# Kernel optimization log

Measured on AMD Instinct MI355X. Metric: run time of the kernel, lower is better.

## Reference

```python
import jax, jax.numpy as jnp
import numpy as np

N = 50000   # nodes
E = 800000  # edges per layer
D = 128     # feature dim
H = 256     # mlp hidden
O = 3       # output dim


def setup_inputs() -> dict:
    key = jax.random.key(0)
    ks = jax.random.split(key, 16)
    def lin(k, fan_out, fan_in):
        s = 1.0 / np.sqrt(fan_in)
        kw, kb = jax.random.split(k)
        return (jax.random.uniform(kw, (fan_out, fan_in), jnp.float32, -s, s),
                jax.random.uniform(kb, (fan_out,), jnp.float32, -s, s))
    x = jax.random.normal(ks[0], (N, D), jnp.float32)
    edge_idx0 = jax.random.randint(ks[1], (2, E), 0, N, dtype=jnp.int64)
    edge_idx1 = jax.random.randint(ks[2], (2, E), 0, N, dtype=jnp.int64)
    Wl1, bl1 = lin(ks[3], D, D)   # SAGE layer1: lin_l (aggregated neighbors, with bias)
    Wr1, _ = lin(ks[4], D, D)     # SAGE layer1: lin_r (root, no bias)
    Wl2, bl2 = lin(ks[5], D, D)
    Wr2, _ = lin(ks[6], D, D)
    Ws, bs = lin(ks[7], D, D)     # skip_fc
    W1, b1 = lin(ks[8], H, D)     # mlp hidden
    W2, b2 = lin(ks[9], O, H)     # mlp out
    return dict(x=x, edge_idx0=edge_idx0, edge_idx1=edge_idx1,
                Wl1=Wl1, bl1=bl1, Wr1=Wr1, Wl2=Wl2, bl2=bl2, Wr2=Wr2,
                Ws=Ws, bs=bs, W1=W1, b1=b1, W2=W2, b2=b2)


def _sage(x, ei, Wl, bl, Wr):
    # PyG SAGEConv with mean aggregation: out = lin_l(mean_j x_j) + lin_r(x_i)
    src, dst = ei[0], ei[1]
    agg = jax.ops.segment_sum(x[src], dst, num_segments=N)          # [N, D] gather-scatter
    cnt = jax.ops.segment_sum(jnp.ones((ei.shape[1],), x.dtype), dst, num_segments=N)
    agg = agg / jnp.maximum(cnt, 1.0)[:, None]
    return agg @ Wl.T + bl + x @ Wr.T


def reference(x, edge_idx0, edge_idx1, Wl1, bl1, Wr1, Wl2, bl2, Wr2,
              Ws, bs, W1, b1, W2, b2):
    inp = x
    h = _sage(x, edge_idx0, Wl1, bl1, Wr1)
    h = _sage(h, edge_idx1, Wl2, bl2, Wr2)
    h = h + (inp @ Ws.T + bs)            # skip connection
    h = jax.nn.relu(h @ W1.T + b1)       # MLP head
    return h @ W2.T + b2                  # [N, 3]
```

## Files before the change

### kernel.cpp

```cpp
#include <hip/hip_runtime.h>
#include <hip/hip_bf16.h>


#define DD 128
#define SB 8
#define CH 4096
typedef unsigned short u16;
typedef __attribute__((ext_vector_type(8))) short short8;
typedef __attribute__((ext_vector_type(4))) float f32x4;

__device__ inline u16 f2bf(float f) {
    __hip_bfloat16 h = __float2bfloat16(f);
    u16 u;
    __builtin_memcpy(&u, &h, 2);
    return u;
}
__device__ inline unsigned pack2(float lo, float hi) {
    return (unsigned)f2bf(lo) | ((unsigned)f2bf(hi) << 16);
}
__device__ inline float bf_lo(unsigned u) { union { unsigned x; float f; } c; c.x = u << 16; return c.f; }
__device__ inline float bf_hi(unsigned u) { union { unsigned x; float f; } c; c.x = u & 0xffff0000u; return c.f; }

struct CastJobs {
    const float4* src[6];
    uint2* dst[6];
    int qstart[7];
};

__global__ __launch_bounds__(256) void hist1_kernel(CastJobs jb,
                                                    const int* __restrict__ dst0, int* __restrict__ h0,
                                                    const int* __restrict__ dst1, int* __restrict__ h1,
                                                    int e0, int e1, int nb, int P) {
    int bx = blockIdx.x;
    int t = threadIdx.x;
    if (bx >= P) {
        if (blockIdx.y == 0) {
            int q = (bx - P) * 256 + t;
            if (q < jb.qstart[6]) {
                int i = 0;
#pragma unroll
                for (int k = 1; k < 6; ++k) if (q >= jb.qstart[k]) i = k;
                int local = q - jb.qstart[i];
                float4 v = jb.src[i][local];
                jb.dst[i][local] = make_uint2(pack2(v.x, v.y), pack2(v.z, v.w));
            }
        }
        return;
    }
    int arr = blockIdx.y;
    const int* dst = arr ? dst1 : dst0;
    int* hist = arr ? h1 : h0;
    int e = arr ? e1 : e0;
    __shared__ int h[256];
    h[t] = 0;
    __syncthreads();
    int base = bx * CH;
    int hi = min(base + CH, e);
    for (int i = base + t; i < hi; i += 256) atomicAdd(&h[dst[i] >> SB], 1);
    __syncthreads();
    if (t < nb) hist[t * P + bx] = h[t];
}

__global__ __launch_bounds__(256) void rowsum_kernel(const int* __restrict__ h0, int* __restrict__ bs0,
                                                     const int* __restrict__ h1, int* __restrict__ bs1,
                                                     int P) {
    int arr = blockIdx.y;
    const int* hist = arr ? h1 : h0;
    int* bs = arr ? bs1 : bs0;
    int b = blockIdx.x;
    __shared__ int s[256];
    int t = threadIdx.x;
    s[t] = (t < P) ? hist[b * P + t] : 0;
    __syncthreads();
    for (int off = 128; off; off >>= 1) {
        if (t < off) s[t] += s[t + off];
        __syncthreads();
    }
    if (t == 0) bs[b] = s[0];
}

__global__ __launch_bounds__(256) void bscan_kernel(const int* __restrict__ bs0, int* __restrict__ bb0, int* __restrict__ rp0, int e0,
                                                    const int* __restrict__ bs1, int* __restrict__ bb1, int* __restrict__ rp1, int e1,
                                                    int nb, int n) {
    int arr = blockIdx.x;
    const int* bsum = arr ? bs1 : bs0;
    int* bb = arr ? bb1 : bb0;
    int* rp = arr ? rp1 : rp0;
    int E = arr ? e1 : e0;
    __shared__ int s[256];
    int t = threadIdx.x;
    int v = (t < nb) ? bsum[t] : 0;
    s[t] = v;
    __syncthreads();
    for (int off = 1; off < 256; off <<= 1) {
        int u = (t >= off) ? s[t - off] : 0;
        __syncthreads();
        s[t] += u;
        __syncthreads();
    }
    if (t < nb) bb[t] = s[t] - v;
    if (t == 0) { bb[nb] = E; rp[n] = E; }
}

__global__ __launch_bounds__(256) void offs_kernel(int* __restrict__ h0, const int* __restrict__ bb0,
                                                   int* __restrict__ h1, const int* __restrict__ bb1,
                                                   int P) {
    int arr = blockIdx.y;
    int* hist = arr ? h1 : h0;
    const int* bb = arr ? bb1 : bb0;
    int b = blockIdx.x;
    __shared__ int s[256];
    int t = threadIdx.x;
    int v = (t < P) ? hist[b * P + t] : 0;
    s[t] = v;
    __syncthreads();
    for (int off = 1; off < 256; off <<= 1) {
        int u = (t >= off) ? s[t - off] : 0;
        __syncthreads();
        s[t] += u;
        __syncthreads();
    }
    if (t < P) hist[b * P + t] = s[t] - v + bb[b];
}

__global__ __launch_bounds__(256) void scatter1_kernel(
    const int* __restrict__ src0, const int* __restrict__ dst0, const int* __restrict__ h0, unsigned* __restrict__ binned0,
    const int* __restrict__ src1, const int* __restrict__ dst1, const int* __restrict__ h1, unsigned* __restrict__ binned1,
    int e0, int e1, int nb, int P) {
    int arr = blockIdx.y;
    const int* src = arr ? src1 : src0;
    const int* dst = arr ? dst1 : dst0;
    const int* hist = arr ? h1 : h0;
    unsigned* binned = arr ? binned1 : binned0;
    int e = arr ? e1 : e0;
    int p = blockIdx.x;
    __shared__ int cnt[256];
    int t = threadIdx.x;
    if (t < nb) cnt[t] = hist[t * P + p];
    __syncthreads();
    int base = p * CH;
    int hi = min(base + CH, e);
    for (int i = base + t; i < hi; i += 256) {
        int d = dst[i];
        int pos = atomicAdd(&cnt[d >> SB], 1);
        binned[pos] = ((unsigned)d << 16) | (unsigned)src[i];
    }
}

__global__ __launch_bounds__(256) void place_kernel(
    const unsigned* __restrict__ binned0, const int* __restrict__ bb0, int* __restrict__ rp0, u16* __restrict__ csr0,
    const unsigned* __restrict__ binned1, const int* __restrict__ bb1, int* __restrict__ rp1, u16* __restrict__ csr1,
    int n, int nb) {
    int arr = blockIdx.y;
    const unsigned* binned = arr ? binned1 : binned0;
    const int* bb = arr ? bb1 : bb0;
    int* rp = arr ? rp1 : rp0;
    u16* csr = arr ? csr1 : csr0;
    int b = blockIdx.x;
    __shared__ int cnt[256];
    __shared__ int s[256];
    int t = threadIdx.x;
    int base = bb[b], end = bb[b + 1];
    cnt[t] = 0;
    __syncthreads();
    for (int i = base + t; i < end; i += 256)
        atomicAdd(&cnt[(binned[i] >> 16) & 255], 1);
    __syncthreads();
    int deg = cnt[t];
    s[t] = deg;
    __syncthreads();
    for (int off = 1; off < 256; off <<= 1) {
        int u = (t >= off) ? s[t - off] : 0;
        __syncthreads();
        s[t] += u;
        __syncthreads();
    }
    int gpos = base + s[t] - deg;
    int node = (b << SB) + t;
    if (node < n) rp[node] = gpos;
    cnt[t] = gpos;
    __syncthreads();
    for (int i = base + t; i < end; i += 256) {
        unsigned pk = binned[i];
        int ld = (pk >> 16) & 255;
        int pos = atomicAdd(&cnt[ld], 1);
        csr[pos] = (u16)(pk & 0xffffu);
    }
}

__global__ __launch_bounds__(256) void agg1_kernel(const u16* __restrict__ G1,
                                                   const u16* __restrict__ csr,
                                                   const int* __restrict__ rp,
                                                   const float* __restrict__ bl1,
                                                   u16* __restrict__ h1, int n) {
    int g = (blockIdx.x * 256 + threadIdx.x) >> 4;
    int lane = threadIdx.x & 15;
    if (g >= n) return;
    int start = rp[g], end = rp[g + 1];
    int d = end - start;
    const uint4* X4 = (const uint4*)G1;
    float acc[8] = {0.f, 0.f, 0.f, 0.f, 0.f, 0.f, 0.f, 0.f};
    int e = start;
    for (; e + 3 < end; e += 4) {
        int s0 = csr[e], s1 = csr[e + 1], s2 = csr[e + 2], s3 = csr[e + 3];
        uint4 v0 = X4[(size_t)s0 * 48 + lane];
        uint4 v1 = X4[(size_t)s1 * 48 + lane];
        uint4 v2 = X4[(size_t)s2 * 48 + lane];
        uint4 v3 = X4[(size_t)s3 * 48 + lane];
        acc[0] += (bf_lo(v0.x) + bf_lo(v1.x)) + (bf_lo(v2.x) + bf_lo(v3.x));
        acc[1] += (bf_hi(v0.x) + bf_hi(v1.x)) + (bf_hi(v2.x) + bf_hi(v3.x));
        acc[2] += (bf_lo(v0.y) + bf_lo(v1.y)) + (bf_lo(v2.y) + bf_lo(v3.y));
        acc[3] += (bf_hi(v0.y) + bf_hi(v1.y)) + (bf_hi(v2.y) + bf_hi(v3.y));
        acc[4] += (bf_lo(v0.z) + bf_lo(v1.z)) + (bf_lo(v2.z) + bf_lo(v3.z));
        acc[5] += (bf_hi(v0.z) + bf_hi(v1.z)) + (bf_hi(v2.z) + bf_hi(v3.z));
        acc[6] += (bf_lo(v0.w) + bf_lo(v1.w)) + (bf_lo(v2.w) + bf_lo(v3.w));
        acc[7] += (bf_hi(v0.w) + bf_hi(v1.w)) + (bf_hi(v2.w) + bf_hi(v3.w));
    }
    for (; e < end; ++e) {
        uint4 v0 = X4[(size_t)csr[e] * 48 + lane];
        acc[0] += bf_lo(v0.x); acc[1] += bf_hi(v0.x);
        acc[2] += bf_lo(v0.y); acc[3] += bf_hi(v0.y);
        acc[4] += bf_lo(v0.z); acc[5] += bf_hi(v0.z);
        acc[6] += bf_lo(v0.w); acc[7] += bf_hi(v0.w);
    }
    float sc = 1.0f / (float)max(d, 1);
    uint4 m = X4[(size_t)g * 48 + 16 + lane];
    const float4* bl = (const float4*)bl1;
    float4 ba = bl[lane * 2], bb = bl[lane * 2 + 1];
    uint4 r;
    r.x = pack2(acc[0] * sc + bf_lo(m.x) + ba.x, acc[1] * sc + bf_hi(m.x) + ba.y);
    r.y = pack2(acc[2] * sc + bf_lo(m.y) + ba.z, acc[3] * sc + bf_hi(m.y) + ba.w);
    r.z = pack2(acc[4] * sc + bf_lo(m.z) + bb.x, acc[5] * sc + bf_hi(m.z) + bb.y);
    r.w = pack2(acc[6] * sc + bf_lo(m.w) + bb.z, acc[7] * sc + bf_hi(m.w) + bb.w);
    ((uint4*)h1)[(size_t)g * 16 + lane] = r;
}

__global__ __launch_bounds__(256) void agg2_kernel(const u16* __restrict__ G2,
                                                   const u16* __restrict__ G1,
                                                   const u16* __restrict__ csr,
                                                   const int* __restrict__ rp,
                                                   const float* __restrict__ bl2,
                                                   const float* __restrict__ bs,
                                                   u16* __restrict__ h3, int n) {
    int g = (blockIdx.x * 256 + threadIdx.x) >> 4;
    int lane = threadIdx.x & 15;
    if (g >= n) return;
    int start = rp[g], end = rp[g + 1];
    int d = end - start;
    const uint4* X4 = (const uint4*)G2;
    float acc[8] = {0.f, 0.f, 0.f, 0.f, 0.f, 0.f, 0.f, 0.f};
    int e = start;
    for (; e + 3 < end; e += 4) {
        int s0 = csr[e], s1 = csr[e + 1], s2 = csr[e + 2], s3 = csr[e + 3];
        uint4 v0 = X4[(size_t)s0 * 32 + lane];
        uint4 v1 = X4[(size_t)s1 * 32 + lane];
        uint4 v2 = X4[(size_t)s2 * 32 + lane];
        uint4 v3 = X4[(size_t)s3 * 32 + lane];
        acc[0] += (bf_lo(v0.x) + bf_lo(v1.x)) + (bf_lo(v2.x) + bf_lo(v3.x));
        acc[1] += (bf_hi(v0.x) + bf_hi(v1.x)) + (bf_hi(v2.x) + bf_hi(v3.x));
        acc[2] += (bf_lo(v0.y) + bf_lo(v1.y)) + (bf_lo(v2.y) + bf_lo(v3.y));
        acc[3] += (bf_hi(v0.y) + bf_hi(v1.y)) + (bf_hi(v2.y) + bf_hi(v3.y));
        acc[4] += (bf_lo(v0.z) + bf_lo(v1.z)) + (bf_lo(v2.z) + bf_lo(v3.z));
        acc[5] += (bf_hi(v0.z) + bf_hi(v1.z)) + (bf_hi(v2.z) + bf_hi(v3.z));
        acc[6] += (bf_lo(v0.w) + bf_lo(v1.w)) + (bf_lo(v2.w) + bf_lo(v3.w));
        acc[7] += (bf_hi(v0.w) + bf_hi(v1.w)) + (bf_hi(v2.w) + bf_hi(v3.w));
    }
    for (; e < end; ++e) {
        uint4 v0 = X4[(size_t)csr[e] * 32 + lane];
        acc[0] += bf_lo(v0.x); acc[1] += bf_hi(v0.x);
        acc[2] += bf_lo(v0.y); acc[3] += bf_hi(v0.y);
        acc[4] += bf_lo(v0.z); acc[5] += bf_hi(v0.z);
        acc[6] += bf_lo(v0.w); acc[7] += bf_hi(v0.w);
    }
    float sc = 1.0f / (float)max(d, 1);
    uint4 m2 = X4[(size_t)g * 32 + 16 + lane];
    uint4 m1 = ((const uint4*)G1)[(size_t)g * 48 + 32 + lane];
    const float4* c2 = (const float4*)bl2;
    const float4* cs = (const float4*)bs;
    float4 ba = c2[lane * 2], bb = c2[lane * 2 + 1];
    float4 sa = cs[lane * 2], sb = cs[lane * 2 + 1];
    uint4 r;
    r.x = pack2(acc[0] * sc + bf_lo(m2.x) + bf_lo(m1.x) + ba.x + sa.x,
                acc[1] * sc + bf_hi(m2.x) + bf_hi(m1.x) + ba.y + sa.y);
    r.y = pack2(acc[2] * sc + bf_lo(m2.y) + bf_lo(m1.y) + ba.z + sa.z,
                acc[3] * sc + bf_hi(m2.y) + bf_hi(m1.y) + ba.w + sa.w);
    r.z = pack2(acc[4] * sc + bf_lo(m2.z) + bf_lo(m1.z) + bb.x + sb.x,
                acc[5] * sc + bf_hi(m2.z) + bf_hi(m1.z) + bb.y + sb.y);
    r.w = pack2(acc[6] * sc + bf_lo(m2.w) + bf_lo(m1.w) + bb.z + sb.z,
                acc[7] * sc + bf_hi(m2.w) + bf_hi(m1.w) + bb.w + sb.w);
    ((uint4*)h3)[(size_t)g * 16 + lane] = r;
}

template <bool F32A>
__global__ __launch_bounds__(256) void mfma_gemm(const void* __restrict__ Av,
                                                 const u16* __restrict__ W,
                                                 u16* __restrict__ C, int M, int NC) {
    __shared__ u16 Bs[32 * 512];
    const int t = threadIdx.x;
    const int colBase = blockIdx.y * 128;
#pragma unroll
    for (int i = 0; i < 8; ++i) {
        int id = t + 256 * i;
        int nrow = id >> 4, cc = id & 15;
        int f = ((nrow >> 4) << 2) | (cc >> 2);
        int dl = ((cc & 3) << 4) | (nrow & 15);
        *(uint4*)&Bs[(f * 64 + dl) * 8] = ((const uint4*)W)[(size_t)(colBase + nrow) * 16 + cc];
    }
    __syncthreads();
    const int w = t >> 6, lane = t & 63, r = lane & 15, half = lane >> 4;
    short8 bf[32];
#pragma unroll
    for (int f = 0; f < 32; ++f)
        bf[f] = *(const short8*)&Bs[(f * 64 + lane) * 8];
    const int nTiles = M >> 4;
    const int nWaves = gridDim.x * 4;
    for (int tile = blockIdx.x * 4 + w; tile < nTiles; tile += nWaves) {
        int rowA = (tile << 4) + r;
        short8 af[4];
        if (F32A) {
            const float4* Arow = (const float4*)Av + (size_t)rowA * 32 + half * 2;
#pragma unroll
            for (int kk = 0; kk < 4; ++kk) {
                float4 a = Arow[kk * 8], b = Arow[kk * 8 + 1];
                uint4 v = make_uint4(pack2(a.x, a.y), pack2(a.z, a.w),
                                     pack2(b.x, b.y), pack2(b.z, b.w));
                af[kk] = *(short8*)&v;
            }
        } else {
            const uint4* Arow = (const uint4*)Av + (size_t)rowA * 16 + half;
#pragma unroll
            for (int kk = 0; kk < 4; ++kk) {
                uint4 v = Arow[kk * 4];
                af[kk] = *(short8*)&v;
            }
        }
        f32x4 acc[8];
#pragma unroll
        for (int i = 0; i < 8; ++i) acc[i] = (f32x4){0.f, 0.f, 0.f, 0.f};
#pragma unroll
        for (int kk = 0; kk < 4; ++kk)
#pragma unroll
            for (int ct = 0; ct < 8; ++ct)
                acc[ct] = __builtin_amdgcn_mfma_f32_16x16x32_bf16(af[kk], bf[ct * 4 + kk], acc[ct], 0, 0, 0);
#pragma unroll
        for (int ct = 0; ct < 8; ++ct) {
            int col = colBase + ct * 16 + r;
#pragma unroll
            for (int reg = 0; reg < 4; ++reg) {
                int row = (tile << 4) + half * 4 + reg;
                C[(size_t)row * NC + col] = f2bf(acc[ct][reg]);
            }
        }
    }
}

__global__ __launch_bounds__(256) void gemm_out_kernel(const u16* __restrict__ h3,
                                                       const u16* __restrict__ W1,
                                                       const float* __restrict__ b1,
                                                       const float* __restrict__ W2,
                                                       const float* __restrict__ b2,
                                                       float* __restrict__ out, int M) {
    __shared__ u16 Bs[64 * 512];
    __shared__ float w2s[3 * 256];
    __shared__ float b1s[256];
    const int t = threadIdx.x;
#pragma unroll
    for (int i = 0; i < 16; ++i) {
        int id = t + 256 * i;
        int nrow = id >> 4, cc = id & 15;
        int f = ((nrow >> 4) << 2) | (cc >> 2);
        int dl = ((cc & 3) << 4) | (nrow & 15);
        *(uint4*)&Bs[(f * 64 + dl) * 8] = ((const uint4*)W1)[(size_t)nrow * 16 + cc];
    }
    for (int i = t; i < 768; i += 256) w2s[i] = W2[i];
    b1s[t] = b1[t];
    __syncthreads();
    const int w = t >> 6, lane = t & 63, r = lane & 15, half = lane >> 4;
    const int nTiles = M >> 4;
    const int nWaves = gridDim.x * 4;
    const u16* bB = &Bs[lane * 8];
    float c0 = b2[0], c1 = b2[1], c2 = b2[2];
    for (int tile = blockIdx.x * 4 + w; tile < nTiles; tile += nWaves) {
        int rowA = (tile << 4) + r;
        const uint4* Arow = (const uint4*)h3 + (size_t)rowA * 16 + half;
        short8 af[4];
#pragma unroll
        for (int kk = 0; kk < 4; ++kk) {
            uint4 v = Arow[kk * 4];
            af[kk] = *(short8*)&v;
        }
        f32x4 acc[16];
#pragma unroll
        for (int i = 0; i < 16; ++i) acc[i] = (f32x4){0.f, 0.f, 0.f, 0.f};
#pragma unroll
        for (int kk = 0; kk < 4; ++kk)
#pragma unroll
            for (int ct = 0; ct < 16; ++ct) {
                short8 bf = *(const short8*)(bB + (ct * 4 + kk) * 512);
                acc[ct] = __builtin_amdgcn_mfma_f32_16x16x32_bf16(af[kk], bf, acc[ct], 0, 0, 0);
            }
        float p[4][3] = {{0.f, 0.f, 0.f}, {0.f, 0.f, 0.f}, {0.f, 0.f, 0.f}, {0.f, 0.f, 0.f}};
#pragma unroll
        for (int ct = 0; ct < 16; ++ct) {
            int col = ct * 16 + r;
            float bv = b1s[col];
            float w0 = w2s[col], w1 = w2s[256 + col], w2v = w2s[512 + col];
#pragma unroll
            for (int reg = 0; reg < 4; ++reg) {
                float h4 = fmaxf(acc[ct][reg] + bv, 0.f);
                p[reg][0] += h4 * w0;
                p[reg][1] += h4 * w1;
                p[reg][2] += h4 * w2v;
            }
        }
#pragma unroll
        for (int m = 1; m < 16; m <<= 1)
#pragma unroll
            for (int reg = 0; reg < 4; ++reg) {
                p[reg][0] += __shfl_xor(p[reg][0], m);
                p[reg][1] += __shfl_xor(p[reg][1], m);
                p[reg][2] += __shfl_xor(p[reg][2], m);
            }
        if (r == 0) {
#pragma unroll
            for (int reg = 0; reg < 4; ++reg) {
                int row = (tile << 4) + half * 4 + reg;
                out[(size_t)row * 3 + 0] = p[reg][0] + c0;
                out[(size_t)row * 3 + 1] = p[reg][1] + c1;
                out[(size_t)row * 3 + 2] = p[reg][2] + c2;
            }
        }
    }
}

extern "C" void kernel_launch(void* const* d_in, const int* in_sizes, int n_in,
                              void* d_out, int out_size, void* d_ws, size_t ws_size,
                              hipStream_t stream) {
    const float* x   = (const float*)d_in[0];
    const int*   ei0 = (const int*)d_in[1];
    const int*   ei1 = (const int*)d_in[2];
    const float* Wl1 = (const float*)d_in[3];
    const float* bl1 = (const float*)d_in[4];
    const float* Wr1 = (const float*)d_in[5];
    const float* Wl2 = (const float*)d_in[6];
    const float* bl2 = (const float*)d_in[7];
    const float* Wr2 = (const float*)d_in[8];
    const float* Wsk = (const float*)d_in[9];
    const float* bsk = (const float*)d_in[10];
    const float* W1  = (const float*)d_in[11];
    const float* b1  = (const float*)d_in[12];
    const float* W2  = (const float*)d_in[13];
    const float* b2  = (const float*)d_in[14];
    float* out = (float*)d_out;

    const int N  = in_sizes[0] / DD;
    const int E0 = in_sizes[1] / 2;
    const int E1 = in_sizes[2] / 2;
    const int H  = in_sizes[12];

    const int* src0 = ei0;      const int* dst0 = ei0 + E0;
    const int* src1 = ei1;      const int* dst1 = ei1 + E1;

    const int nb   = (N + 255) >> SB;
    const int Emax = (E0 > E1) ? E0 : E1;
    const int P    = (Emax + CH - 1) / CH;

    char* wp = (char*)d_ws;
    auto carve = [&](size_t bytes) { char* p = wp; wp += (bytes + 255) & ~(size_t)255; return p; };
    u16* G1   = (u16*)carve((size_t)N * 384 * 2);
    u16* G2   = (u16*)carve((size_t)N * 256 * 2);
    u16* h1h  = (u16*)carve((size_t)N * DD * 2);
    u16* h3h  = (u16*)carve((size_t)N * DD * 2);
    u16* wc1  = (u16*)carve((size_t)384 * DD * 2);
    u16* wc2  = (u16*)carve((size_t)256 * DD * 2);
    u16* w1h  = (u16*)carve((size_t)H * DD * 2);
    int* rp0  = (int*)carve((size_t)(N + 1) * 4);
    int* rp1  = (int*)carve((size_t)(N + 1) * 4);
    u16* csr0 = (u16*)carve((size_t)E0 * 2);
    u16* csr1 = (u16*)carve((size_t)E1 * 2);
    unsigned* binned0 = (unsigned*)carve((size_t)E0 * 4);
    unsigned* binned1 = (unsigned*)carve((size_t)E1 * 4);
    int* hist1_0 = (int*)carve((size_t)nb * P * 4);
    int* hist1_1 = (int*)carve((size_t)nb * P * 4);
    int* bsum0 = (int*)carve((size_t)nb * 4);
    int* bsum1 = (int*)carve((size_t)nb * 4);
    int* bb0 = (int*)carve((size_t)(nb + 1) * 4);
    int* bb1 = (int*)carve((size_t)(nb + 1) * 4);

    CastJobs jb;
    const float* srcs[6] = {Wl1, Wr1, Wsk, Wl2, Wr2, W1};
    u16* dsts[6] = {wc1, wc1 + 128 * DD, wc1 + 256 * DD, wc2, wc2 + 128 * DD, w1h};
    int  cnts[6] = {DD * DD, DD * DD, DD * DD, DD * DD, DD * DD, H * DD};
    int q = 0;
    for (int i = 0; i < 6; ++i) {
        jb.src[i] = (const float4*)srcs[i];
        jb.dst[i] = (uint2*)dsts[i];
        jb.qstart[i] = q;
        q += cnts[i] / 4;
    }
    jb.qstart[6] = q;
    const int CB = (q + 255) / 256;

    const int gAgg = (N * 16 + 255) / 256;

    hist1_kernel<<<dim3(P + CB, 2), 256, 0, stream>>>(jb, dst0, hist1_0, dst1, hist1_1, E0, E1, nb, P);
    rowsum_kernel<<<dim3(nb, 2), 256, 0, stream>>>(hist1_0, bsum0, hist1_1, bsum1, P);
    bscan_kernel<<<2, 256, 0, stream>>>(bsum0, bb0, rp0, E0, bsum1, bb1, rp1, E1, nb, N);
    offs_kernel<<<dim3(nb, 2), 256, 0, stream>>>(hist1_0, bb0, hist1_1, bb1, P);
    scatter1_kernel<<<dim3(P, 2), 256, 0, stream>>>(src0, dst0, hist1_0, binned0,
                                                    src1, dst1, hist1_1, binned1, E0, E1, nb, P);
    place_kernel<<<dim3(nb, 2), 256, 0, stream>>>(binned0, bb0, rp0, csr0,
                                                  binned1, bb1, rp1, csr1, N, nb);

    mfma_gemm<true><<<dim3(320, 3), 256, 0, stream>>>(x, wc1, G1, N, 384);
    agg1_kernel<<<gAgg, 256, 0, stream>>>(G1, csr0, rp0, bl1, h1h, N);
    mfma_gemm<false><<<dim3(320, 2), 256, 0, stream>>>(h1h, wc2, G2, N, 256);
    agg2_kernel<<<gAgg, 256, 0, stream>>>(G2, G1, csr1, rp1, bl2, bsk, h3h, N);
    gemm_out_kernel<<<512, 256, 0, stream>>>(h3h, w1h, b1, W2, b2, out, N);
}
```

Baseline: 253.2 us.

## Merge CSR-build scan kernels and widen aggregation to 32 lanes per node

Replaces the rowsum/bscan/offs kernel chain with one per-bin scan kernel, and recomputes the small bin-sum prefix scan redundantly inside each scatter and place block. This removes two kernel launches and their serialization from the CSR build. The aggregation kernels now use 32 lanes per node with 8-byte loads instead of 16 lanes with 16-byte loads, which doubles the thread count and raises memory-level parallelism for the gather at the cost of narrower per-lane loads. The redundant scans add some per-block work in the scatter and place kernels.

```diff
diff --git a/kernel.cpp b/kernel.cpp
--- a/kernel.cpp
+++ b/kernel.cpp
@@ -61,53 +61,12 @@
     if (t < nb) hist[t * P + bx] = h[t];
 }
 
-__global__ __launch_bounds__(256) void rowsum_kernel(const int* __restrict__ h0, int* __restrict__ bs0,
-                                                     const int* __restrict__ h1, int* __restrict__ bs1,
-                                                     int P) {
-    int arr = blockIdx.y;
-    const int* hist = arr ? h1 : h0;
-    int* bs = arr ? bs1 : bs0;
-    int b = blockIdx.x;
-    __shared__ int s[256];
-    int t = threadIdx.x;
-    s[t] = (t < P) ? hist[b * P + t] : 0;
-    __syncthreads();
-    for (int off = 128; off; off >>= 1) {
-        if (t < off) s[t] += s[t + off];
-        __syncthreads();
-    }
-    if (t == 0) bs[b] = s[0];
-}
-
-__global__ __launch_bounds__(256) void bscan_kernel(const int* __restrict__ bs0, int* __restrict__ bb0, int* __restrict__ rp0, int e0,
-                                                    const int* __restrict__ bs1, int* __restrict__ bb1, int* __restrict__ rp1, int e1,
-                                                    int nb, int n) {
-    int arr = blockIdx.x;
-    const int* bsum = arr ? bs1 : bs0;
-    int* bb = arr ? bb1 : bb0;
-    int* rp = arr ? rp1 : rp0;
-    int E = arr ? e1 : e0;
-    __shared__ int s[256];
-    int t = threadIdx.x;
-    int v = (t < nb) ? bsum[t] : 0;
-    s[t] = v;
-    __syncthreads();
-    for (int off = 1; off < 256; off <<= 1) {
-        int u = (t >= off) ? s[t - off] : 0;
-        __syncthreads();
-        s[t] += u;
-        __syncthreads();
-    }
-    if (t < nb) bb[t] = s[t] - v;
-    if (t == 0) { bb[nb] = E; rp[n] = E; }
-}
-
-__global__ __launch_bounds__(256) void offs_kernel(int* __restrict__ h0, const int* __restrict__ bb0,
-                                                   int* __restrict__ h1, const int* __restrict__ bb1,
+__global__ __launch_bounds__(256) void scan_kernel(int* __restrict__ h0, int* __restrict__ bs0,
+                                                   int* __restrict__ h1, int* __restrict__ bs1,
                                                    int P) {
     int arr = blockIdx.y;
     int* hist = arr ? h1 : h0;
-    const int* bb = arr ? bb1 : bb0;
+    int* bs = arr ? bs1 : bs0;
     int b = blockIdx.x;
     __shared__ int s[256];
     int t = threadIdx.x;
@@ -120,23 +79,37 @@
         s[t] += u;
         __syncthreads();
     }
-    if (t < P) hist[b * P + t] = s[t] - v + bb[b];
+    if (t < P) hist[b * P + t] = s[t] - v;
+    if (t == 0) bs[b] = s[255];
 }
 
 __global__ __launch_bounds__(256) void scatter1_kernel(
-    const int* __restrict__ src0, const int* __restrict__ dst0, const int* __restrict__ h0, unsigned* __restrict__ binned0,
-    const int* __restrict__ src1, const int* __restrict__ dst1, const int* __restrict__ h1, unsigned* __restrict__ binned1,
+    const int* __restrict__ src0, const int* __restrict__ dst0, const int* __restrict__ h0,
+    const int* __restrict__ bs0, unsigned* __restrict__ binned0,
+    const int* __restrict__ src1, const int* __restrict__ dst1, const int* __restrict__ h1,
+    const int* __restrict__ bs1, unsigned* __restrict__ binned1,
     int e0, int e1, int nb, int P) {
     int arr = blockIdx.y;
     const int* src = arr ? src1 : src0;
     const int* dst = arr ? dst1 : dst0;
     const int* hist = arr ? h1 : h0;
+    const int* bs = arr ? bs1 : bs0;
     unsigned* binned = arr ? binned1 : binned0;
     int e = arr ? e1 : e0;
     int p = blockIdx.x;
     __shared__ int cnt[256];
+    __shared__ int s[256];
     int t = threadIdx.x;
-    if (t < nb) cnt[t] = hist[t * P + p];
+    int v = (t < nb) ? bs[t] : 0;
+    s[t] = v;
+    __syncthreads();
+    for (int off = 1; off < 256; off <<= 1) {
+        int u = (t >= off) ? s[t - off] : 0;
+        __syncthreads();
+        s[t] += u;
+        __syncthreads();
+    }
+    if (t < nb) cnt[t] = hist[t * P + p] + (s[t] - v);
     __syncthreads();
     int base = p * CH;
     int hi = min(base + CH, e);
@@ -148,19 +121,31 @@
 }
 
 __global__ __launch_bounds__(256) void place_kernel(
-    const unsigned* __restrict__ binned0, const int* __restrict__ bb0, int* __restrict__ rp0, u16* __restrict__ csr0,
-    const unsigned* __restrict__ binned1, const int* __restrict__ bb1, int* __restrict__ rp1, u16* __restrict__ csr1,
-    int n, int nb) {
+    const unsigned* __restrict__ binned0, const int* __restrict__ bs0, int* __restrict__ rp0, u16* __restrict__ csr0,
+    const unsigned* __restrict__ binned1, const int* __restrict__ bs1, int* __restrict__ rp1, u16* __restrict__ csr1,
+    int e0, int e1, int n, int nb) {
     int arr = blockIdx.y;
     const unsigned* binned = arr ? binned1 : binned0;
-    const int* bb = arr ? bb1 : bb0;
+    const int* bs = arr ? bs1 : bs0;
     int* rp = arr ? rp1 : rp0;
     u16* csr = arr ? csr1 : csr0;
+    int E = arr ? e1 : e0;
     int b = blockIdx.x;
     __shared__ int cnt[256];
     __shared__ int s[256];
     int t = threadIdx.x;
-    int base = bb[b], end = bb[b + 1];
+    s[t] = (t < nb) ? bs[t] : 0;
+    __syncthreads();
+    for (int off = 1; off < 256; off <<= 1) {
+        int u = (t >= off) ? s[t - off] : 0;
+        __syncthreads();
+        s[t] += u;
+        __syncthreads();
+    }
+    int base = (b > 0) ? s[b - 1] : 0;
+    int end = s[b];
+    if (b == nb - 1 && t == 0) rp[n] = E;
+    __syncthreads();
     cnt[t] = 0;
     __syncthreads();
     for (int i = base + t; i < end; i += 256)
@@ -193,46 +178,37 @@
                                                    const int* __restrict__ rp,
                                                    const float* __restrict__ bl1,
                                                    u16* __restrict__ h1, int n) {
-    int g = (blockIdx.x * 256 + threadIdx.x) >> 4;
-    int lane = threadIdx.x & 15;
+    int g = (blockIdx.x * 256 + threadIdx.x) >> 5;
+    int lane = threadIdx.x & 31;
     if (g >= n) return;
     int start = rp[g], end = rp[g + 1];
     int d = end - start;
-    const uint4* X4 = (const uint4*)G1;
-    float acc[8] = {0.f, 0.f, 0.f, 0.f, 0.f, 0.f, 0.f, 0.f};
+    const uint2* X2 = (const uint2*)G1;
+    float a0 = 0.f, a1 = 0.f, a2 = 0.f, a3 = 0.f;
     int e = start;
     for (; e + 3 < end; e += 4) {
         int s0 = csr[e], s1 = csr[e + 1], s2 = csr[e + 2], s3 = csr[e + 3];
-        uint4 v0 = X4[(size_t)s0 * 48 + lane];
-        uint4 v1 = X4[(size_t)s1 * 48 + lane];
-        uint4 v2 = X4[(size_t)s2 * 48 + lane];
-        uint4 v3 = X4[(size_t)s3 * 48 + lane];
-        acc[0] += (bf_lo(v0.x) + bf_lo(v1.x)) + (bf_lo(v2.x) + bf_lo(v3.x));
-        acc[1] += (bf_hi(v0.x) + bf_hi(v1.x)) + (bf_hi(v2.x) + bf_hi(v3.x));
-        acc[2] += (bf_lo(v0.y) + bf_lo(v1.y)) + (bf_lo(v2.y) + bf_lo(v3.y));
-        acc[3] += (bf_hi(v0.y) + bf_hi(v1.y)) + (bf_hi(v2.y) + bf_hi(v3.y));
-        acc[4] += (bf_lo(v0.z) + bf_lo(v1.z)) + (bf_lo(v2.z) + bf_lo(v3.z));
-        acc[5] += (bf_hi(v0.z) + bf_hi(v1.z)) + (bf_hi(v2.z) + bf_hi(v3.z));
-        acc[6] += (bf_lo(v0.w) + bf_lo(v1.w)) + (bf_lo(v2.w) + bf_lo(v3.w));
-        acc[7] += (bf_hi(v0.w) + bf_hi(v1.w)) + (bf_hi(v2.w) + bf_hi(v3.w));
+        uint2 v0 = X2[(size_t)s0 * 96 + lane];
+        uint2 v1 = X2[(size_t)s1 * 96 + lane];
+        uint2 v2 = X2[(size_t)s2 * 96 + lane];
+        uint2 v3 = X2[(size_t)s3 * 96 + lane];
+        a0 += (bf_lo(v0.x) + bf_lo(v1.x)) + (bf_lo(v2.x) + bf_lo(v3.x));
+        a1 += (bf_hi(v0.x) + bf_hi(v1.x)) + (bf_hi(v2.x) + bf_hi(v3.x));
+        a2 += (bf_lo(v0.y) + bf_lo(v1.y)) + (bf_lo(v2.y) + bf_lo(v3.y));
+        a3 += (bf_hi(v0.y) + bf_hi(v1.y)) + (bf_hi(v2.y) + bf_hi(v3.y));
     }
     for (; e < end; ++e) {
-        uint4 v0 = X4[(size_t)csr[e] * 48 + lane];
-        acc[0] += bf_lo(v0.x); acc[1] += bf_hi(v0.x);
-        acc[2] += bf_lo(v0.y); acc[3] += bf_hi(v0.y);
-        acc[4] += bf_lo(v0.z); acc[5] += bf_hi(v0.z);
-        acc[6] += bf_lo(v0.w); acc[7] += bf_hi(v0.w);
+        uint2 v0 = X2[(size_t)csr[e] * 96 + lane];
+        a0 += bf_lo(v0.x); a1 += bf_hi(v0.x);
+        a2 += bf_lo(v0.y); a3 += bf_hi(v0.y);
     }
     float sc = 1.0f / (float)max(d, 1);
-    uint4 m = X4[(size_t)g * 48 + 16 + lane];
-    const float4* bl = (const float4*)bl1;
-    float4 ba = bl[lane * 2], bb = bl[lane * 2 + 1];
-    uint4 r;
-    r.x = pack2(acc[0] * sc + bf_lo(m.x) + ba.x, acc[1] * sc + bf_hi(m.x) + ba.y);
-    r.y = pack2(acc[2] * sc + bf_lo(m.y) + ba.z, acc[3] * sc + bf_hi(m.y) + ba.w);
-    r.z = pack2(acc[4] * sc + bf_lo(m.z) + bb.x, acc[5] * sc + bf_hi(m.z) + bb.y);
-    r.w = pack2(acc[6] * sc + bf_lo(m.w) + bb.z, acc[7] * sc + bf_hi(m.w) + bb.w);
-    ((uint4*)h1)[(size_t)g * 16 + lane] = r;
+    uint2 m = X2[(size_t)g * 96 + 32 + lane];
+    float4 b = ((const float4*)bl1)[lane];
+    uint2 r;
+    r.x = pack2(a0 * sc + bf_lo(m.x) + b.x, a1 * sc + bf_hi(m.x) + b.y);
+    r.y = pack2(a2 * sc + bf_lo(m.y) + b.z, a3 * sc + bf_hi(m.y) + b.w);
+    ((uint2*)h1)[(size_t)g * 32 + lane] = r;
 }
 
 __global__ __launch_bounds__(256) void agg2_kernel(const u16* __restrict__ G2,
@@ -242,53 +218,41 @@
                                                    const float* __restrict__ bl2,
                                                    const float* __restrict__ bs,
                                                    u16* __restrict__ h3, int n) {
-    int g = (blockIdx.x * 256 + threadIdx.x) >> 4;
-    int lane = threadIdx.x & 15;
+    int g = (blockIdx.x * 256 + threadIdx.x) >> 5;
+    int lane = threadIdx.x & 31;
     if (g >= n) return;
     int start = rp[g], end = rp[g + 1];
     int d = end - start;
-    const uint4* X4 = (const uint4*)G2;
-    float acc[8] = {0.f, 0.f, 0.f, 0.f, 0.f, 0.f, 0.f, 0.f};
+    const uint2* X2 = (const uint2*)G2;
+    float a0 = 0.f, a1 = 0.f, a2 = 0.f, a3 = 0.f;
     int e = start;
     for (; e + 3 < end; e += 4) {
         int s0 = csr[e], s1 = csr[e + 1], s2 = csr[e + 2], s3 = csr[e + 3];
-        uint4 v0 = X4[(size_t)s0 * 32 + lane];
-        uint4 v1 = X4[(size_t)s1 * 32 + lane];
-        uint4 v2 = X4[(size_t)s2 * 32 + lane];
-        uint4 v3 = X4[(size_t)s3 * 32 + lane];
-        acc[0] += (bf_lo(v0.x) + bf_lo(v1.x)) + (bf_lo(v2.x) + bf_lo(v3.x));
-        acc[1] += (bf_hi(v0.x) + bf_hi(v1.x)) + (bf_hi(v2.x) + bf_hi(v3.x));
-        acc[2] += (bf_lo(v0.y) + bf_lo(v1.y)) + (bf_lo(v2.y) + bf_lo(v3.y));
-        acc[3] += (bf_hi(v0.y) + bf_hi(v1.y)) + (bf_hi(v2.y) + bf_hi(v3.y));
-        acc[4] += (bf_lo(v0.z) + bf_lo(v1.z)) + (bf_lo(v2.z) + bf_lo(v3.z));
-        acc[5] += (bf_hi(v0.z) + bf_hi(v1.z)) + (bf_hi(v2.z) + bf_hi(v3.z));
-        acc[6] += (bf_lo(v0.w) + bf_lo(v1.w)) + (bf_lo(v2.w) + bf_lo(v3.w));
-        acc[7] += (bf_hi(v0.w) + bf_hi(v1.w)) + (bf_hi(v2.w) + bf_hi(v3.w));
+        uint2 v0 = X2[(size_t)s0 * 64 + lane];
+        uint2 v1 = X2[(size_t)s1 * 64 + lane];
+        uint2 v2 = X2[(size_t)s2 * 64 + lane];
+        uint2 v3 = X2[(size_t)s3 * 64 + lane];
+        a0 += (bf_lo(v0.x) + bf_lo(v1.x)) + (bf_lo(v2.x) + bf_lo(v3.x));
+        a1 += (bf_hi(v0.x) + bf_hi(v1.x)) + (bf_hi(v2.x) + bf_hi(v3.x));
+        a2 += (bf_lo(v0.y) + bf_lo(v1.y)) + (bf_lo(v2.y) + bf_lo(v3.y));
+        a3 += (bf_hi(v0.y) + bf_hi(v1.y)) + (bf_hi(v2.y) + bf_hi(v3.y));
     }
     for (; e < end; ++e) {
-        uint4 v0 = X4[(size_t)csr[e] * 32 + lane];
-        acc[0] += bf_lo(v0.x); acc[1] += bf_hi(v0.x);
-        acc[2] += bf_lo(v0.y); acc[3] += bf_hi(v0.y);
-        acc[4] += bf_lo(v0.z); acc[5] += bf_hi(v0.z);
-        acc[6] += bf_lo(v0.w); acc[7] += bf_hi(v0.w);
+        uint2 v0 = X2[(size_t)csr[e] * 64 + lane];
+        a0 += bf_lo(v0.x); a1 += bf_hi(v0.x);
+        a2 += bf_lo(v0.y); a3 += bf_hi(v0.y);
     }
     float sc = 1.0f / (float)max(d, 1);
-    uint4 m2 = X4[(size_t)g * 32 + 16 + lane];
-    uint4 m1 = ((const uint4*)G1)[(size_t)g * 48 + 32 + lane];
-    const float4* c2 = (const float4*)bl2;
-    const float4* cs = (const float4*)bs;
-    float4 ba = c2[lane * 2], bb = c2[lane * 2 + 1];
-    float4 sa = cs[lane * 2], sb = cs[lane * 2 + 1];
-    uint4 r;
-    r.x = pack2(acc[0] * sc + bf_lo(m2.x) + bf_lo(m1.x) + ba.x + sa.x,
-                acc[1] * sc + bf_hi(m2.x) + bf_hi(m1.x) + ba.y + sa.y);
-    r.y = pack2(acc[2] * sc + bf_lo(m2.y) + bf_lo(m1.y) + ba.z + sa.z,
-                acc[3] * sc + bf_hi(m2.y) + bf_hi(m1.y) + ba.w + sa.w);
-    r.z = pack2(acc[4] * sc + bf_lo(m2.z) + bf_lo(m1.z) + bb.x + sb.x,
-                acc[5] * sc + bf_hi(m2.z) + bf_hi(m1.z) + bb.y + sb.y);
-    r.w = pack2(acc[6] * sc + bf_lo(m2.w) + bf_lo(m1.w) + bb.z + sb.z,
-                acc[7] * sc + bf_hi(m2.w) + bf_hi(m1.w) + bb.w + sb.w);
-    ((uint4*)h3)[(size_t)g * 16 + lane] = r;
+    uint2 m2 = X2[(size_t)g * 64 + 32 + lane];
+    uint2 m1 = ((const uint2*)G1)[(size_t)g * 96 + 64 + lane];
+    float4 cb = ((const float4*)bl2)[lane];
+    float4 sb = ((const float4*)bs)[lane];
+    uint2 r;
+    r.x = pack2(a0 * sc + bf_lo(m2.x) + bf_lo(m1.x) + cb.x + sb.x,
+                a1 * sc + bf_hi(m2.x) + bf_hi(m1.x) + cb.y + sb.y);
+    r.y = pack2(a2 * sc + bf_lo(m2.y) + bf_lo(m1.y) + cb.z + sb.z,
+                a3 * sc + bf_hi(m2.y) + bf_hi(m1.y) + cb.w + sb.w);
+    ((uint2*)h3)[(size_t)g * 32 + lane] = r;
 }
 
 template <bool F32A>
@@ -484,8 +448,6 @@
     int* hist1_1 = (int*)carve((size_t)nb * P * 4);
     int* bsum0 = (int*)carve((size_t)nb * 4);
     int* bsum1 = (int*)carve((size_t)nb * 4);
-    int* bb0 = (int*)carve((size_t)(nb + 1) * 4);
-    int* bb1 = (int*)carve((size_t)(nb + 1) * 4);
 
     CastJobs jb;
     const float* srcs[6] = {Wl1, Wr1, Wsk, Wl2, Wr2, W1};
@@ -501,16 +463,14 @@
     jb.qstart[6] = q;
     const int CB = (q + 255) / 256;
 
-    const int gAgg = (N * 16 + 255) / 256;
+    const int gAgg = (N * 32 + 255) / 256;
 
     hist1_kernel<<<dim3(P + CB, 2), 256, 0, stream>>>(jb, dst0, hist1_0, dst1, hist1_1, E0, E1, nb, P);
-    rowsum_kernel<<<dim3(nb, 2), 256, 0, stream>>>(hist1_0, bsum0, hist1_1, bsum1, P);
-    bscan_kernel<<<2, 256, 0, stream>>>(bsum0, bb0, rp0, E0, bsum1, bb1, rp1, E1, nb, N);
-    offs_kernel<<<dim3(nb, 2), 256, 0, stream>>>(hist1_0, bb0, hist1_1, bb1, P);
-    scatter1_kernel<<<dim3(P, 2), 256, 0, stream>>>(src0, dst0, hist1_0, binned0,
-                                                    src1, dst1, hist1_1, binned1, E0, E1, nb, P);
-    place_kernel<<<dim3(nb, 2), 256, 0, stream>>>(binned0, bb0, rp0, csr0,
-                                                  binned1, bb1, rp1, csr1, N, nb);
+    scan_kernel<<<dim3(nb, 2), 256, 0, stream>>>(hist1_0, bsum0, hist1_1, bsum1, P);
+    scatter1_kernel<<<dim3(P, 2), 256, 0, stream>>>(src0, dst0, hist1_0, bsum0, binned0,
+                                                    src1, dst1, hist1_1, bsum1, binned1, E0, E1, nb, P);
+    place_kernel<<<dim3(nb, 2), 256, 0, stream>>>(binned0, bsum0, rp0, csr0,
+                                                  binned1, bsum1, rp1, csr1, E0, E1, N, nb);
 
     mfma_gemm<true><<<dim3(320, 3), 256, 0, stream>>>(x, wc1, G1, N, 384);
     agg1_kernel<<<gAgg, 256, 0, stream>>>(G1, csr0, rp0, bl1, h1h, N);
```

New measurement: 256.2 us. About the same (+1.2%).
